# Optimization experiments

Hardware: AMD Instinct MI355X
Metric: run time of the kernel (lower is better)

## Reference

```python
import jax, jax.numpy as jnp
import numpy as np

B, H, W, N, C = 2, 56, 56, 2, 128
NUM_HEADS = 8
SPLIT = 7
IDX = 0  # 0 -> H_sp = H, W_sp = split_size (vertical stripes)


def setup_inputs() -> dict:
    key = jax.random.key(0)
    k1, k2, k3, k4 = jax.random.split(key, 4)
    query = jax.random.normal(k1, (B, H, W, N, C), jnp.float32)
    key_t = jax.random.normal(k2, (B, H, W, N, C), jnp.float32)
    value = jax.random.normal(k3, (B, H, W, N, C), jnp.float32)
    conv_w = jax.random.normal(k4, (C, 1, 3, 3), jnp.float32) * 0.1  # depthwise get_v weight
    return {"query": query, "key": key_t, "value": value, "conv_w": conv_w}


def _im2cswin(x, Hsp, Wsp, h):
    # [b, Hp, Wp, n, c] -> [(b i j), h, Hsp*Wsp*n, d]
    b, Hp, Wp, n, c = x.shape
    i, j = Hp // Hsp, Wp // Wsp
    d = c // h
    x = x.reshape(b, i, Hsp, j, Wsp, n, h, d)
    x = x.transpose(0, 1, 3, 6, 2, 4, 5, 7)  # b i j h Hsp Wsp n d
    return x.reshape(b * i * j, h, Hsp * Wsp * n, d)


def _window_mask(Hsp, Wsp, n):
    # block attention between same spatial position / different candidates (except diagonal)
    pos = jnp.repeat(jnp.arange(Hsp * Wsp), n)
    L = pos.shape[0]
    m = jnp.where(pos[:, None] == pos[None, :], -jnp.inf, 0.0).astype(jnp.float32)
    m = m.at[jnp.arange(L), jnp.arange(L)].set(0.0)
    return m


def reference(query, key, value, conv_w):
    b, Hh, Ww, n, c = query.shape
    if IDX == -1:
        Hsp, Wsp = Hh, Ww
    elif IDX == 0:
        Hsp, Wsp = Hh, SPLIT
    else:
        Hsp, Wsp = SPLIT, Ww
    # H % Hsp == 0 and W % Wsp == 0 by construction -> no padding branch
    h = NUM_HEADS
    d = c // h
    scale = d ** (-0.5)

    q = _im2cswin(query, Hsp, Wsp, h)
    k = _im2cswin(key, Hsp, Wsp, h)
    v = _im2cswin(value, Hsp, Wsp, h)

    # rpe via depthwise 3x3 conv over the value (LePE-style), summed over candidates
    v_img = value.transpose(0, 3, 4, 1, 2).reshape(b * n, c, Hh, Ww)  # [b*n, C, H, W]
    conv = jax.lax.conv_general_dilated(
        v_img, conv_w, (1, 1), 'SAME',
        dimension_numbers=('NCHW', 'OIHW', 'NCHW'), feature_group_count=c)
    rpe = conv.reshape(b, n, c, Hh, Ww).sum(1, keepdims=True)
    center = conv_w[:, 0, 1, 1]  # center tap of each depthwise kernel
    self_scaled = (v_img * center[None, :, None, None]).reshape(b, n, c, Hh, Ww)
    self_scaled = self_scaled - self_scaled.sum(1, keepdims=True)
    rpe = (rpe + self_scaled).transpose(0, 3, 4, 1, 2)  # [b, H, W, n, c]

    mask = _window_mask(Hsp, Wsp, n)[None, None]  # [1,1,L,L]
    attn = jnp.einsum('bhid,bhjd->bhij', q * scale, k) + mask
    attn = jax.nn.softmax(attn.astype(jnp.float32), axis=-1).astype(q.dtype)
    x = jnp.einsum('bhij,bhjd->bhid', attn, v)

    # windows back to image layout
    i, j = Hh // Hsp, Ww // Wsp
    x = x.reshape(b, i, j, h, Hsp, Wsp, n, d)
    x = x.transpose(0, 1, 4, 2, 5, 6, 3, 7).reshape(b, Hh, Ww, n, c)
    return x + rpe
```

## Files before the change

kernel.cpp:

```cpp
#include <hip/hip_runtime.h>

typedef __bf16 bf16x8 __attribute__((ext_vector_type(8)));
typedef float f32x16 __attribute__((ext_vector_type(16)));
typedef unsigned u32x2 __attribute__((ext_vector_type(2)));

#define BB 2
#define HH 56
#define WW 56
#define NN 2
#define CC 128
#define NH 8
#define DD 16
#define WSP 7
#define LQ 784
#define KB_TOK 800
#define VT_STRIDE 808
#define NKC 25
#define NINST 128
#define BPI 5
#define NWAVE 5
#define YSTRIP 7
#define NB_RPE 448
#define YSTRD 14336
#define BSTRD 802816

#define QSCALE 0.3606737602222409f

union U2 { __bf16 h[2]; unsigned u; };
union U4 { unsigned u[4]; bf16x8 v; };
union H8 { bf16x8 v; uint4 q; };

__global__ __launch_bounds__(256) void rpe_kernel(const float* __restrict__ value,
                                                  const float* __restrict__ conv_w,
                                                  float* __restrict__ out) {
    const int bx = blockIdx.x;
    const int tid = threadIdx.x;
    const int b     = bx / 224;
    const int r0    = bx - b * 224;
    const int strip = r0 / 28;
    const int blk   = r0 - strip * 28;
    const int idx   = blk * 256 + tid;
    const int c     = idx & 127;
    const int x     = idx >> 7;
    const int y0    = strip * YSTRIP;

    float w[9];
#pragma unroll
    for (int k = 0; k < 9; ++k) w[k] = conv_w[c * 9 + k];
    const float center = w[4];

    const float* vb = value + (long)b * BSTRD + x * (NN * CC) + c;
    float* ob = out + (long)b * BSTRD + x * (NN * CC) + c;
    const bool xm = x > 0, xp = x < WW - 1;

    auto loadS = [&](int y, int dx) -> float {
        const float* p = vb + y * YSTRD + dx * (NN * CC);
        return p[0] + p[CC];
    };

    float sm[3], s0[3], sp[3];
    if (y0 > 0) {
        sm[0] = xm ? loadS(y0 - 1, -1) : 0.f;
        sm[1] = loadS(y0 - 1, 0);
        sm[2] = xp ? loadS(y0 - 1, 1) : 0.f;
    } else { sm[0] = sm[1] = sm[2] = 0.f; }
    s0[0] = xm ? loadS(y0, -1) : 0.f;
    s0[1] = loadS(y0, 0);
    s0[2] = xp ? loadS(y0, 1) : 0.f;

#pragma unroll
    for (int yy = 0; yy < YSTRIP; ++yy) {
        const int y = y0 + yy;
        if (y + 1 < HH) {
            sp[0] = xm ? loadS(y + 1, -1) : 0.f;
            sp[1] = loadS(y + 1, 0);
            sp[2] = xp ? loadS(y + 1, 1) : 0.f;
        } else { sp[0] = sp[1] = sp[2] = 0.f; }

        float conv_sum = w[0] * sm[0] + w[1] * sm[1] + w[2] * sm[2]
                       + w[3] * s0[0] + w[4] * s0[1] + w[5] * s0[2]
                       + w[6] * sp[0] + w[7] * sp[1] + w[8] * sp[2];
        float v0 = vb[y * YSTRD];
        float v1 = s0[1] - v0;
        float base = conv_sum - center * s0[1];
        float* po = ob + y * YSTRD;
        po[0]  = base + center * v0;
        po[CC] = base + center * v1;

        sm[0] = s0[0]; sm[1] = s0[1]; sm[2] = s0[2];
        s0[0] = sp[0]; s0[1] = sp[1]; s0[2] = sp[2];
    }
}

__global__ __launch_bounds__(320) void attn_fused(const float* __restrict__ q_g,
                                                  const float* __restrict__ k_g,
                                                  const float* __restrict__ v_g,
                                                  float* __restrict__ out) {
    __shared__ alignas(16) __bf16 Klds[KB_TOK * 16];
    __shared__ alignas(16) __bf16 Vlds[17 * VT_STRIDE];

    const int bid  = blockIdx.x;
    const int g    = bid >> 3;
    const int inst = (bid & 7) + 8 * (g / BPI);
    const int part = g % BPI;
    const int head = inst & 7;
    const int win  = inst >> 3;
    const int b    = win >> 3, wj = win & 7;

    const int tid  = threadIdx.x;

    for (int tok = tid; tok < KB_TOK; tok += 320) {
        Vlds[16 * VT_STRIDE + tok] = (__bf16)1.f;
        if (tok < LQ) {
            int pos = tok >> 1, n = tok & 1;
            int y = pos / WSP, xl = pos - y * WSP;
            long off = ((long)(((b * HH + y) * WW + wj * WSP + xl) * NN + n)) * CC + head * DD;

            float kv[16], vv[16];
            *(float4*)&kv[0]  = *(const float4*)(k_g + off);
            *(float4*)&kv[4]  = *(const float4*)(k_g + off + 4);
            *(float4*)&kv[8]  = *(const float4*)(k_g + off + 8);
            *(float4*)&kv[12] = *(const float4*)(k_g + off + 12);
            *(float4*)&vv[0]  = *(const float4*)(v_g + off);
            *(float4*)&vv[4]  = *(const float4*)(v_g + off + 4);
            *(float4*)&vv[8]  = *(const float4*)(v_g + off + 8);
            *(float4*)&vv[12] = *(const float4*)(v_g + off + 12);

            H8 lo, hi;
#pragma unroll
            for (int i = 0; i < 8; ++i) { lo.v[i] = (__bf16)kv[i]; hi.v[i] = (__bf16)kv[8 + i]; }
            *(uint4*)&Klds[tok * 16]     = lo.q;
            *(uint4*)&Klds[tok * 16 + 8] = hi.q;
#pragma unroll
            for (int d = 0; d < 16; ++d)
                Vlds[d * VT_STRIDE + tok] = (__bf16)vv[d];
        } else {
            H8 z; z.q = make_uint4(0, 0, 0, 0);
            *(uint4*)&Klds[tok * 16]     = z.q;
            *(uint4*)&Klds[tok * 16 + 8] = z.q;
#pragma unroll
            for (int d = 0; d < 16; ++d)
                Vlds[d * VT_STRIDE + tok] = (__bf16)0.f;
        }
    }
    __syncthreads();

    const int w    = tid >> 6;
    const int lane = tid & 63;
    const int col  = lane & 31;
    const int h    = lane >> 5;
    const int qt   = part * NWAVE + w;
    const int myq  = qt * 32 + col;
    const int sib  = myq ^ 1;

    const int myqc = myq < LQ ? myq : LQ - 1;
    const int pos = myqc >> 1, n = myqc & 1;
    const int y = pos / WSP, xl = pos - y * WSP;
    const long ooff = ((long)(((b * HH + y) * WW + wj * WSP + xl) * NN + n)) * CC + head * DD;

    bf16x8 qfv;
    {
        const float* qp = q_g + ooff + 8 * h;
        float qv[8];
        *(float4*)&qv[0] = *(const float4*)qp;
        *(float4*)&qv[4] = *(const float4*)(qp + 4);
        H8 qq;
#pragma unroll
        for (int i = 0; i < 8; ++i) qq.v[i] = (__bf16)(qv[i] * QSCALE);
        qfv = qq.v;
    }

    f32x16 acc, zv;
#pragma unroll
    for (int i = 0; i < 16; ++i) { acc[i] = 0.f; zv[i] = 0.f; }

    const char* kbase = (const char*)Klds + col * 32 + h * 16;
    const int vrow = col < 16 ? col : 16;
    const char* vbase = (const char*)Vlds + vrow * (VT_STRIDE * 2) + h * 16;

    for (int c = 0; c < NKC; ++c) {
        bf16x8 kf = *(const bf16x8*)(kbase + c * 1024);

        f32x16 st = __builtin_amdgcn_mfma_f32_32x32x16_bf16(kf, qfv, zv, 0, 0, 0);

        float p[16];
        if (c == qt || c == NKC - 1) {
#pragma unroll
            for (int r = 0; r < 16; ++r) {
                int kr = (r & 3) + 8 * (r >> 2) + 4 * h;
                int gk = c * 32 + kr;
                p[r] = (gk >= LQ || gk == sib) ? 0.f : __builtin_amdgcn_exp2f(st[r]);
            }
        } else {
#pragma unroll
            for (int r = 0; r < 16; ++r) p[r] = __builtin_amdgcn_exp2f(st[r]);
        }

        unsigned pk[4][2];
#pragma unroll
        for (int b2 = 0; b2 < 4; ++b2) {
            U2 a, bb;
            a.h[0]  = (__bf16)p[4 * b2 + 0];
            a.h[1]  = (__bf16)p[4 * b2 + 1];
            bb.h[0] = (__bf16)p[4 * b2 + 2];
            bb.h[1] = (__bf16)p[4 * b2 + 3];
            pk[b2][0] = a.u;
            pk[b2][1] = bb.u;
        }

#pragma unroll
        for (int t = 0; t < 2; ++t) {
            U4 pb;
#pragma unroll
            for (int j = 0; j < 2; ++j) {
#if __has_builtin(__builtin_amdgcn_permlane32_swap)
                u32x2 rr = __builtin_amdgcn_permlane32_swap(pk[2 * t][j], pk[2 * t + 1][j], false, false);
                pb.u[j]     = rr[0];
                pb.u[2 + j] = rr[1];
#else
                unsigned swa = __shfl_xor(pk[2 * t][j], 32, 64);
                unsigned swb = __shfl_xor(pk[2 * t + 1][j], 32, 64);
                pb.u[j]     = h ? swb : pk[2 * t][j];
                pb.u[2 + j] = h ? pk[2 * t + 1][j] : swa;
#endif
            }
            bf16x8 vf = *(const bf16x8*)(vbase + c * 64 + t * 32);
            acc = __builtin_amdgcn_mfma_f32_32x32x16_bf16(vf, pb.v, acc, 0, 0, 0);
        }
    }

    if (myq < LQ) {
        float inv = 1.f / acc[8];
        float* po = out + ooff;
        float4 r0 = *(float4*)(po + 4 * h);
        r0.x += acc[0] * inv; r0.y += acc[1] * inv;
        r0.z += acc[2] * inv; r0.w += acc[3] * inv;
        *(float4*)(po + 4 * h) = r0;
        float4 r1 = *(float4*)(po + 8 + 4 * h);
        r1.x += acc[4] * inv; r1.y += acc[5] * inv;
        r1.z += acc[6] * inv; r1.w += acc[7] * inv;
        *(float4*)(po + 8 + 4 * h) = r1;
    }
}

extern "C" void kernel_launch(void* const* d_in, const int* in_sizes, int n_in,
                              void* d_out, int out_size, void* d_ws, size_t ws_size,
                              hipStream_t stream) {
    const float* q = (const float*)d_in[0];
    const float* k = (const float*)d_in[1];
    const float* v = (const float*)d_in[2];
    const float* w = (const float*)d_in[3];
    float* out = (float*)d_out;

    rpe_kernel<<<NB_RPE, 256, 0, stream>>>(v, w, out);

    attn_fused<<<NINST * BPI, 320, 0, stream>>>(q, k, v, out);
}
```

Measured before the change: 44.81 us.

## Fuse depthwise-conv RPE into attention epilogue, drop separate rpe kernel

Removes the standalone rpe_kernel and computes the 3x3 depthwise conv plus self-scaled correction per query inside the attention kernel's epilogue. Conv weights for the head are staged in LDS, and the ones-row for the softmax denominator moves from the V^T tile to a small shared buffer. This removes one launch and the read-modify-write of the output. In exchange, each query re-reads 9 neighbor value vectors from global/L2, which is redundant work, and the epilogue grows longer.

```diff
diff --git a/kernel.cpp b/kernel.cpp
--- a/kernel.cpp
+++ b/kernel.cpp
@@ -19,10 +19,12 @@
 #define NINST 128
 #define BPI 5
 #define NWAVE 5
-#define YSTRIP 7
-#define NB_RPE 448
-#define YSTRD 14336
-#define BSTRD 802816
+
+#define K_OFF 0
+#define V_OFF 25600
+#define W_OFF 51456
+#define ONES_OFF 52032
+#define SMEM_BYTES 52064
 
 #define QSCALE 0.3606737602222409f
 
@@ -30,74 +32,24 @@
 union U4 { unsigned u[4]; bf16x8 v; };
 union H8 { bf16x8 v; uint4 q; };
 
-__global__ __launch_bounds__(256) void rpe_kernel(const float* __restrict__ value,
-                                                  const float* __restrict__ conv_w,
-                                                  float* __restrict__ out) {
-    const int bx = blockIdx.x;
-    const int tid = threadIdx.x;
-    const int b     = bx / 224;
-    const int r0    = bx - b * 224;
-    const int strip = r0 / 28;
-    const int blk   = r0 - strip * 28;
-    const int idx   = blk * 256 + tid;
-    const int c     = idx & 127;
-    const int x     = idx >> 7;
-    const int y0    = strip * YSTRIP;
-
-    float w[9];
-#pragma unroll
-    for (int k = 0; k < 9; ++k) w[k] = conv_w[c * 9 + k];
-    const float center = w[4];
-
-    const float* vb = value + (long)b * BSTRD + x * (NN * CC) + c;
-    float* ob = out + (long)b * BSTRD + x * (NN * CC) + c;
-    const bool xm = x > 0, xp = x < WW - 1;
-
-    auto loadS = [&](int y, int dx) -> float {
-        const float* p = vb + y * YSTRD + dx * (NN * CC);
-        return p[0] + p[CC];
-    };
-
-    float sm[3], s0[3], sp[3];
-    if (y0 > 0) {
-        sm[0] = xm ? loadS(y0 - 1, -1) : 0.f;
-        sm[1] = loadS(y0 - 1, 0);
-        sm[2] = xp ? loadS(y0 - 1, 1) : 0.f;
-    } else { sm[0] = sm[1] = sm[2] = 0.f; }
-    s0[0] = xm ? loadS(y0, -1) : 0.f;
-    s0[1] = loadS(y0, 0);
-    s0[2] = xp ? loadS(y0, 1) : 0.f;
-
-#pragma unroll
-    for (int yy = 0; yy < YSTRIP; ++yy) {
-        const int y = y0 + yy;
-        if (y + 1 < HH) {
-            sp[0] = xm ? loadS(y + 1, -1) : 0.f;
-            sp[1] = loadS(y + 1, 0);
-            sp[2] = xp ? loadS(y + 1, 1) : 0.f;
-        } else { sp[0] = sp[1] = sp[2] = 0.f; }
-
-        float conv_sum = w[0] * sm[0] + w[1] * sm[1] + w[2] * sm[2]
-                       + w[3] * s0[0] + w[4] * s0[1] + w[5] * s0[2]
-                       + w[6] * sp[0] + w[7] * sp[1] + w[8] * sp[2];
-        float v0 = vb[y * YSTRD];
-        float v1 = s0[1] - v0;
-        float base = conv_sum - center * s0[1];
-        float* po = ob + y * YSTRD;
-        po[0]  = base + center * v0;
-        po[CC] = base + center * v1;
-
-        sm[0] = s0[0]; sm[1] = s0[1]; sm[2] = s0[2];
-        s0[0] = sp[0]; s0[1] = sp[1]; s0[2] = sp[2];
-    }
+static __device__ __forceinline__ float4 f4zero() { float4 r; r.x = r.y = r.z = r.w = 0.f; return r; }
+static __device__ __forceinline__ float4 f4add(float4 a, float4 b) {
+    float4 r; r.x = a.x + b.x; r.y = a.y + b.y; r.z = a.z + b.z; r.w = a.w + b.w; return r;
+}
+static __device__ __forceinline__ float4 f4fma(float4 acc, float4 w, float4 s) {
+    acc.x += w.x * s.x; acc.y += w.y * s.y; acc.z += w.z * s.z; acc.w += w.w * s.w; return acc;
 }
 
 __global__ __launch_bounds__(320) void attn_fused(const float* __restrict__ q_g,
                                                   const float* __restrict__ k_g,
                                                   const float* __restrict__ v_g,
+                                                  const float* __restrict__ conv_w,
                                                   float* __restrict__ out) {
-    __shared__ alignas(16) __bf16 Klds[KB_TOK * 16];
-    __shared__ alignas(16) __bf16 Vlds[17 * VT_STRIDE];
+    __shared__ alignas(16) char smem[SMEM_BYTES];
+    __bf16* Klds = (__bf16*)(smem + K_OFF);
+    __bf16* Vlds = (__bf16*)(smem + V_OFF);
+    float*  wlds = (float*)(smem + W_OFF);
+    __bf16* onesb = (__bf16*)(smem + ONES_OFF);
 
     const int bid  = blockIdx.x;
     const int g    = bid >> 3;
@@ -106,15 +58,20 @@
     const int head = inst & 7;
     const int win  = inst >> 3;
     const int b    = win >> 3, wj = win & 7;
-
     const int tid  = threadIdx.x;
 
+    if (tid < 144) {
+        int c = tid & 15, k = tid >> 4;
+        wlds[k * 16 + c] = conv_w[(head * 16 + c) * 9 + k];
+    } else if (tid < 160) {
+        onesb[tid - 144] = (__bf16)1.f;
+    }
+
     for (int tok = tid; tok < KB_TOK; tok += 320) {
-        Vlds[16 * VT_STRIDE + tok] = (__bf16)1.f;
         if (tok < LQ) {
             int pos = tok >> 1, n = tok & 1;
-            int y = pos / WSP, xl = pos - y * WSP;
-            long off = ((long)(((b * HH + y) * WW + wj * WSP + xl) * NN + n)) * CC + head * DD;
+            int y = pos / WSP, xl2 = pos - y * WSP;
+            long off = ((long)(((b * HH + y) * WW + wj * WSP + xl2) * NN + n)) * CC + head * DD;
 
             float kv[16], vv[16];
             *(float4*)&kv[0]  = *(const float4*)(k_g + off);
@@ -175,8 +132,15 @@
     for (int i = 0; i < 16; ++i) { acc[i] = 0.f; zv[i] = 0.f; }
 
     const char* kbase = (const char*)Klds + col * 32 + h * 16;
-    const int vrow = col < 16 ? col : 16;
-    const char* vbase = (const char*)Vlds + vrow * (VT_STRIDE * 2) + h * 16;
+    const char* vbase;
+    int vstep, tstep;
+    if (col < 16) {
+        vbase = (const char*)Vlds + col * (VT_STRIDE * 2) + h * 16;
+        vstep = 64; tstep = 32;
+    } else {
+        vbase = (const char*)onesb;
+        vstep = 0; tstep = 0;
+    }
 
     for (int c = 0; c < NKC; ++c) {
         bf16x8 kf = *(const bf16x8*)(kbase + c * 1024);
@@ -224,21 +188,60 @@
                 pb.u[2 + j] = h ? pk[2 * t + 1][j] : swa;
 #endif
             }
-            bf16x8 vf = *(const bf16x8*)(vbase + c * 64 + t * 32);
+            bf16x8 vf = *(const bf16x8*)(vbase + c * vstep + t * tstep);
             acc = __builtin_amdgcn_mfma_f32_32x32x16_bf16(vf, pb.v, acc, 0, 0, 0);
         }
     }
 
     if (myq < LQ) {
+        const int xg = wj * WSP + xl;
+        const long rowbase = ((long)(b * HH + y) * WW + xg) * (NN * CC) + head * DD;
+
+        float4 cv0 = f4zero(), cv1 = f4zero();
+        float4 sc0 = f4zero(), sc1 = f4zero();
+        float4 vn0 = f4zero(), vn1 = f4zero();
+
+#pragma unroll
+        for (int dy = -1; dy <= 1; ++dy) {
+            int yy = y + dy;
+#pragma unroll
+            for (int dx = -1; dx <= 1; ++dx) {
+                int xx = xg + dx;
+                if (yy < 0 || yy >= HH || xx < 0 || xx >= WW) continue;
+                int k = (dy + 1) * 3 + (dx + 1);
+                const float* p = v_g + rowbase + ((long)dy * WW + dx) * (NN * CC);
+                float4 a0 = *(const float4*)(p + 4 * h);
+                float4 b0 = *(const float4*)(p + CC + 4 * h);
+                float4 a1 = *(const float4*)(p + 8 + 4 * h);
+                float4 b1 = *(const float4*)(p + CC + 8 + 4 * h);
+                float4 w0 = *(const float4*)(wlds + k * 16 + 4 * h);
+                float4 w1 = *(const float4*)(wlds + k * 16 + 8 + 4 * h);
+                float4 S0 = f4add(a0, b0);
+                float4 S1 = f4add(a1, b1);
+                cv0 = f4fma(cv0, w0, S0);
+                cv1 = f4fma(cv1, w1, S1);
+                if (dy == 0 && dx == 0) {
+                    sc0 = S0; sc1 = S1;
+                    vn0 = n ? b0 : a0;
+                    vn1 = n ? b1 : a1;
+                }
+            }
+        }
+        float4 wc0 = *(const float4*)(wlds + 4 * 16 + 4 * h);
+        float4 wc1 = *(const float4*)(wlds + 4 * 16 + 8 + 4 * h);
+
         float inv = 1.f / acc[8];
         float* po = out + ooff;
-        float4 r0 = *(float4*)(po + 4 * h);
-        r0.x += acc[0] * inv; r0.y += acc[1] * inv;
-        r0.z += acc[2] * inv; r0.w += acc[3] * inv;
+        float4 r0, r1;
+        r0.x = cv0.x + wc0.x * (vn0.x - sc0.x) + acc[0] * inv;
+        r0.y = cv0.y + wc0.y * (vn0.y - sc0.y) + acc[1] * inv;
+        r0.z = cv0.z + wc0.z * (vn0.z - sc0.z) + acc[2] * inv;
+        r0.w = cv0.w + wc0.w * (vn0.w - sc0.w) + acc[3] * inv;
+        r1.x = cv1.x + wc1.x * (vn1.x - sc1.x) + acc[4] * inv;
+        r1.y = cv1.y + wc1.y * (vn1.y - sc1.y) + acc[5] * inv;
+        r1.z = cv1.z + wc1.z * (vn1.z - sc1.z) + acc[6] * inv;
+        r1.w = cv1.w + wc1.w * (vn1.w - sc1.w) + acc[7] * inv;
         *(float4*)(po + 4 * h) = r0;
-        float4 r1 = *(float4*)(po + 8 + 4 * h);
-        r1.x += acc[4] * inv; r1.y += acc[5] * inv;
-        r1.z += acc[6] * inv; r1.w += acc[7] * inv;
         *(float4*)(po + 8 + 4 * h) = r1;
     }
 }
@@ -252,7 +255,5 @@
     const float* w = (const float*)d_in[3];
     float* out = (float*)d_out;
 
-    rpe_kernel<<<NB_RPE, 256, 0, stream>>>(v, w, out);
-
-    attn_fused<<<NINST * BPI, 320, 0, stream>>>(q, k, v, out);
-}
+    attn_fused<<<NINST * BPI, 320, 0, stream>>>(q, k, v, w, out);
+}
```

Result: faster. 37.71 us (-15.8%).
